# Optimization experiments

Hardware: AMD Instinct MI355X
Metric: run time of the kernel (lower is better)

## Reference

```python
import jax, jax.numpy as jnp
import numpy as np

DIM = 1024
HEADS = 16
HEAD_DIM = DIM // HEADS
MLP = 4 * DIM
EPS = 1e-5


def layer_norm(x, g, b):
    mu = jnp.mean(x, axis=-1, keepdims=True)
    var = jnp.var(x, axis=-1, keepdims=True)
    return (x - mu) * jax.lax.rsqrt(var + EPS) * g + b


def rope_cos_sin(n, d):
    inv_freq = 1.0 / (10000.0 ** (jnp.arange(0, d, 2, dtype=jnp.float32) / d))
    t = jnp.arange(n, dtype=jnp.float32)
    freqs = jnp.outer(t, inv_freq)          # [N, d/2]
    emb = jnp.concatenate([freqs, freqs], -1)  # [N, d]
    return jnp.cos(emb), jnp.sin(emb)


def rotate_half(x):
    x1, x2 = x[..., ::2], x[..., 1::2]
    return jnp.concatenate([-x2, x1], axis=-1)


def setup_inputs() -> dict:
    key = jax.random.key(0)
    ks = jax.random.split(key, 16)
    B, N = 2, 2048
    s = lambda fan_in: 1.0 / np.sqrt(fan_in)
    inp = {
        "x": jax.random.normal(ks[0], (B, N, DIM), jnp.float32),
        "t_emb": jax.random.normal(ks[1], (B, DIM), jnp.float32),
        "norm1_g": jnp.ones((DIM,), jnp.float32),
        "norm1_b": jnp.zeros((DIM,), jnp.float32),
        "Wq": jax.random.normal(ks[2], (DIM, DIM), jnp.float32) * s(DIM),
        "Wk": jax.random.normal(ks[3], (DIM, DIM), jnp.float32) * s(DIM),
        "Wv": jax.random.normal(ks[4], (DIM, DIM), jnp.float32) * s(DIM),
        "Wo": jax.random.normal(ks[5], (DIM, DIM), jnp.float32) * s(DIM),
        "norm2_g": jnp.ones((DIM,), jnp.float32),
        "norm2_b": jnp.zeros((DIM,), jnp.float32),
        "W1": jax.random.normal(ks[6], (DIM, MLP), jnp.float32) * s(DIM),
        "W2": jax.random.normal(ks[7], (MLP, DIM), jnp.float32) * s(MLP),
        "ada_W": jax.random.normal(ks[8], (DIM, 6 * DIM), jnp.float32) * s(DIM),
        "ada_b": jnp.zeros((6 * DIM,), jnp.float32),
    }
    return inp


def reference(x, t_emb, norm1_g, norm1_b, Wq, Wk, Wv, Wo,
              norm2_g, norm2_b, W1, W2, ada_W, ada_b):
    B, N, C = x.shape
    H, D = HEADS, HEAD_DIM
    scale = D ** -0.5

    mod = jax.nn.silu(t_emb) @ ada_W + ada_b          # [B, 6C]
    (shift_msa, scale_msa, gate_msa,
     shift_mlp, scale_mlp, gate_mlp) = jnp.split(mod, 6, axis=-1)

    xn = layer_norm(x, norm1_g, norm1_b) * (1 + scale_msa[:, None, :]) + shift_msa[:, None, :]

    q = (xn @ Wq).reshape(B, N, H, D).transpose(0, 2, 1, 3)  # [B,H,N,D]
    k = (xn @ Wk).reshape(B, N, H, D).transpose(0, 2, 1, 3)
    v = (xn @ Wv).reshape(B, N, H, D).transpose(0, 2, 1, 3)

    cos, sin = rope_cos_sin(N, D)                     # [N, D]
    q = q * cos + rotate_half(q) * sin
    k = k * cos + rotate_half(k) * sin

    attn = jnp.einsum('bhnd,bhmd->bhnm', q, k) * scale  # explicit O(N^2) scores
    attn = jax.nn.softmax(attn, axis=-1)
    out = jnp.einsum('bhnm,bhmd->bhnd', attn, v)

    out = out.transpose(0, 2, 1, 3).reshape(B, N, C) @ Wo
    x = x + gate_msa[:, None, :] * out

    xn = layer_norm(x, norm2_g, norm2_b) * (1 + scale_mlp[:, None, :]) + shift_mlp[:, None, :]
    mlp = jax.nn.gelu(xn @ W1, approximate=False) @ W2
    x = x + gate_mlp[:, None, :] * mlp
    return x
```

## Files before the change

### kernel.cpp

```cpp
#include <hip/hip_runtime.h>
#include <math.h>

#define BB    2
#define NN    2048
#define CDIM  1024
#define HEADS 16
#define HDIM  64
#define MLPD  4096
#define MODC  6144
#define EPSV  1e-5f
#define LOG2E 1.4426950408889634f
#define MSPLIT 16

typedef __attribute__((ext_vector_type(8))) short s8v;
typedef __attribute__((ext_vector_type(4))) float f4v;

__device__ inline unsigned short f2bf(float f) {
  union { float f; unsigned u; } v; v.f = f;
  unsigned r = v.u + 0x7FFFu + ((v.u >> 16) & 1u);
  return (unsigned short)(r >> 16);
}
__device__ inline float bf2f(unsigned short h) {
  union { unsigned u; float f; } v; v.u = ((unsigned)h) << 16;
  return v.f;
}

__global__ __launch_bounds__(256) void mod_part(
    const float* __restrict__ t_emb, const float* __restrict__ ada_W,
    float* __restrict__ part) {
  int j = blockIdx.x * 256 + threadIdx.x;
  int b = blockIdx.y, ks = blockIdx.z;
  __shared__ float st[64];
  if (threadIdx.x < 64) {
    float v = t_emb[b * CDIM + ks * 64 + threadIdx.x];
    st[threadIdx.x] = v / (1.0f + expf(-v));
  }
  __syncthreads();
  float acc = 0.f;
  const float* wp = ada_W + (size_t)(ks * 64) * MODC + j;
  #pragma unroll 8
  for (int i = 0; i < 64; ++i) acc += st[i] * wp[(size_t)i * MODC];
  part[((size_t)ks * BB + b) * MODC + j] = acc;
}

__global__ __launch_bounds__(256) void mod_reduce(
    const float* __restrict__ part, const float* __restrict__ ada_b,
    float* __restrict__ mod) {
  int idx = blockIdx.x * 256 + threadIdx.x;
  int b = idx / MODC, j = idx % MODC;
  float a = ada_b[j];
  #pragma unroll
  for (int s = 0; s < MSPLIT; ++s) a += part[((size_t)s * BB + b) * MODC + j];
  mod[(size_t)b * MODC + j] = a;
}

__device__ inline float wave_sum64(float v) {
  for (int o = 32; o > 0; o >>= 1) v += __shfl_down(v, o, 64);
  return v;
}

__global__ __launch_bounds__(256) void ln_mod_bf16(
    const float* __restrict__ x, const float* __restrict__ g,
    const float* __restrict__ bta, const float* __restrict__ mod,
    int shift_off, int scale_off, unsigned short* __restrict__ out) {
  int r = blockIdx.x;
  int b = r / NN;
  int t = threadIdx.x;
  const float* xr = x + (size_t)r * CDIM;
  float4 xv = ((const float4*)xr)[t];
  float s  = xv.x + xv.y + xv.z + xv.w;
  float s2 = xv.x*xv.x + xv.y*xv.y + xv.z*xv.z + xv.w*xv.w;
  __shared__ float ws1[4], ws2[4];
  float sw = wave_sum64(s), s2w = wave_sum64(s2);
  int lane = t & 63, wid = t >> 6;
  if (lane == 0) { ws1[wid] = sw; ws2[wid] = s2w; }
  __syncthreads();
  float mu  = (ws1[0] + ws1[1] + ws1[2] + ws1[3]) * (1.0f / CDIM);
  float var = (ws2[0] + ws2[1] + ws2[2] + ws2[3]) * (1.0f / CDIM) - mu * mu;
  float rstd = rsqrtf(var + EPSV);
  const float* mods = mod + (size_t)b * MODC;
  float4 gv = ((const float4*)g)[t];
  float4 bv = ((const float4*)bta)[t];
  float4 sc = ((const float4*)(mods + scale_off))[t];
  float4 sh = ((const float4*)(mods + shift_off))[t];
  ushort4 ov;
  ov.x = f2bf(((xv.x - mu) * rstd * gv.x + bv.x) * (1.0f + sc.x) + sh.x);
  ov.y = f2bf(((xv.y - mu) * rstd * gv.y + bv.y) * (1.0f + sc.y) + sh.y);
  ov.z = f2bf(((xv.z - mu) * rstd * gv.z + bv.z) * (1.0f + sc.z) + sh.z);
  ov.w = f2bf(((xv.w - mu) * rstd * gv.w + bv.w) * (1.0f + sc.w) + sh.w);
  ((ushort4*)(out + (size_t)r * CDIM))[t] = ov;
}

__global__ __launch_bounds__(256) void wcast_all(
    const float* __restrict__ Wq, const float* __restrict__ Wk,
    const float* __restrict__ Wv, const float* __restrict__ Wo,
    const float* __restrict__ W1, const float* __restrict__ W2,
    unsigned short* __restrict__ Wqkvt, unsigned short* __restrict__ Wot,
    unsigned short* __restrict__ W1t, unsigned short* __restrict__ W2t) {
  int bid = blockIdx.x;
  const float* W; unsigned short* Wt; int K, N, t;
  if (bid < 4096) {
    int m = bid >> 10;
    t = bid & 1023;
    K = CDIM; N = CDIM;
    W  = (m == 0) ? Wq : (m == 1) ? Wk : (m == 2) ? Wv : Wo;
    Wt = (m == 3) ? Wot : (Wqkvt + (size_t)m * CDIM * CDIM);
  } else if (bid < 8192) {
    t = bid - 4096; K = CDIM; N = MLPD; W = W1; Wt = W1t;
  } else {
    t = bid - 8192; K = MLPD; N = CDIM; W = W2; Wt = W2t;
  }
  int ntiles = N >> 5;
  int n0 = (t % ntiles) * 32, k0 = (t / ntiles) * 32;
  __shared__ float tile[32][33];
  int tx = threadIdx.x & 31, ty = threadIdx.x >> 5;
  #pragma unroll
  for (int p = 0; p < 4; ++p)
    tile[ty + p * 8][tx] = W[(size_t)(k0 + ty + p * 8) * N + n0 + tx];
  __syncthreads();
  #pragma unroll
  for (int p = 0; p < 4; ++p)
    Wt[(size_t)(n0 + ty + p * 8) * K + k0 + tx] = f2bf(tile[tx][ty + p * 8]);
}

__global__ __launch_bounds__(256) void mfma_gemm(
    const unsigned short* __restrict__ A,
    const unsigned short* __restrict__ Bt,
    int M, int N, int K,
    unsigned short* __restrict__ Ob, unsigned short* __restrict__ Ob2,
    unsigned short* __restrict__ Ob3, int mode) {
  __shared__ unsigned short As[128 * 32];
  __shared__ unsigned short Bs[128 * 32];
  int tid = threadIdx.x;
  int wave = tid >> 6, lane = tid & 63;
  int quad = lane >> 4, l15 = lane & 15;
  int m0 = blockIdx.y * 128, n0 = blockIdx.x * 128;
  int wm = (wave >> 1) * 64, wn = (wave & 1) * 64;

  f4v acc[4][4] = {};
  int srow = lane >> 2;
  int scol = (lane & 3) * 8;

  for (int k0 = 0; k0 < K; k0 += 32) {
    __syncthreads();
    #pragma unroll
    for (int s = 0; s < 2; ++s) {
      int inst = 2 * wave + s;
      const unsigned short* ga =
          A + (size_t)(m0 + inst * 16 + srow) * K + k0 + scol;
      __builtin_amdgcn_global_load_lds(
          (const __attribute__((address_space(1))) unsigned int*)(const void*)ga,
          (__attribute__((address_space(3))) unsigned int*)(void*)(As + inst * 512),
          16, 0, 0);
      const unsigned short* gb =
          Bt + (size_t)(n0 + inst * 16 + srow) * K + k0 + scol;
      __builtin_amdgcn_global_load_lds(
          (const __attribute__((address_space(1))) unsigned int*)(const void*)gb,
          (__attribute__((address_space(3))) unsigned int*)(void*)(Bs + inst * 512),
          16, 0, 0);
    }
    __syncthreads();

    s8v af[4], bf[4];
    #pragma unroll
    for (int i = 0; i < 4; ++i)
      af[i] = *(const s8v*)(As + ((wm + i * 16 + l15) * 32 + quad * 8));
    #pragma unroll
    for (int j = 0; j < 4; ++j)
      bf[j] = *(const s8v*)(Bs + ((wn + j * 16 + l15) * 32 + quad * 8));
    #pragma unroll
    for (int i = 0; i < 4; ++i)
      #pragma unroll
      for (int j = 0; j < 4; ++j)
        acc[i][j] = __builtin_amdgcn_mfma_f32_16x16x32_bf16(
            af[i], bf[j], acc[i][j], 0, 0, 0);
  }

  #pragma unroll
  for (int i = 0; i < 4; ++i) {
    int rbase = m0 + wm + i * 16 + quad * 4;
    #pragma unroll
    for (int j = 0; j < 4; ++j) {
      int c = n0 + wn + j * 16 + l15;
      #pragma unroll
      for (int rg = 0; rg < 4; ++rg) {
        int r = rbase + rg;
        float v = acc[i][j][rg];
        if (mode == 0) {
          unsigned short* dst = (c < 1024) ? Ob : ((c < 2048) ? Ob2 : Ob3);
          dst[(size_t)r * 1024 + (c & 1023)] = f2bf(v);
        } else {
          v = 0.5f * v * (1.0f + erff(v * 0.70710678118f));
          Ob[(size_t)r * N + c] = f2bf(v);
        }
      }
    }
  }
}

__global__ __launch_bounds__(1024) void mfma_gemm_res(
    const unsigned short* __restrict__ A,
    const unsigned short* __restrict__ Bt,
    int M, int N, int K,
    float* __restrict__ O0,
    const float* __restrict__ res, const float* __restrict__ mod,
    int gate_off) {
  __shared__ unsigned short SH[3 * 16384];
  int tid = threadIdx.x;
  int wave = tid >> 6, lane = tid & 63;
  int quad = lane >> 4, l15 = lane & 15;
  int m0 = blockIdx.y * 128, n0 = blockIdx.x * 128;
  int pos = wave & 7;
  int om = pos >> 1, on = pos & 1;
  int ks = wave >> 3;

  f4v acc[2][4] = {};

  int srow = lane >> 3;
  int ksrc = ((lane & 7) ^ (lane >> 3)) << 3;
  const int nt = K >> 6;

  #define STAGE_RES(T, BUF)                                                    \
    {                                                                          \
      int k0_ = (T) << 6;                                                      \
      unsigned short* dsta = SH + (BUF) * 16384 + wave * 512;                  \
      const unsigned short* ga =                                               \
          A + (size_t)(m0 + 8 * wave + srow) * K + k0_ + ksrc;                 \
      __builtin_amdgcn_global_load_lds(                                        \
          (const __attribute__((address_space(1))) unsigned int*)(const void*)ga, \
          (__attribute__((address_space(3))) unsigned int*)(void*)dsta,        \
          16, 0, 0);                                                           \
      const unsigned short* gb =                                               \
          Bt + (size_t)(n0 + 8 * wave + srow) * K + k0_ + ksrc;                \
      __builtin_amdgcn_global_load_lds(                                        \
          (const __attribute__((address_space(1))) unsigned int*)(const void*)gb, \
          (__attribute__((address_space(3))) unsigned int*)(void*)(dsta + 8192), \
          16, 0, 0);                                                           \
    }

  STAGE_RES(0, 0);
  STAGE_RES(1, 1);
  asm volatile("s_waitcnt vmcnt(2)" ::: "memory");
  __syncthreads();

  int kx = (ks * 32 + quad * 8) ^ ((l15 & 7) << 3);

  int rbuf = 0, sbuf = 2;
  for (int t = 0; t < nt; ++t) {
    if (t + 2 < nt) STAGE_RES(t + 2, sbuf);

    const unsigned short* base = SH + rbuf * 16384;
    s8v af[2], bf[4];
    #pragma unroll
    for (int i = 0; i < 2; ++i)
      af[i] = *(const s8v*)(base + (om * 32 + i * 16 + l15) * 64 + kx);
    #pragma unroll
    for (int j = 0; j < 4; ++j)
      bf[j] = *(const s8v*)(base + 8192 + (on * 64 + j * 16 + l15) * 64 + kx);
    #pragma unroll
    for (int i = 0; i < 2; ++i)
      #pragma unroll
      for (int j = 0; j < 4; ++j)
        acc[i][j] = __builtin_amdgcn_mfma_f32_16x16x32_bf16(
            af[i], bf[j], acc[i][j], 0, 0, 0);

    if (t + 2 < nt) {
      asm volatile("s_waitcnt vmcnt(2)" ::: "memory");
    } else if (t + 1 < nt) {
      asm volatile("s_waitcnt vmcnt(0)" ::: "memory");
    }
    __syncthreads();
    rbuf = (rbuf == 2) ? 0 : rbuf + 1;
    sbuf = (sbuf == 2) ? 0 : sbuf + 1;
  }
  #undef STAGE_RES

  float* red = (float*)SH;
  if (wave >= 8) {
    int rb = (wave - 8) * 2304 + lane * 36;
    #pragma unroll
    for (int i = 0; i < 2; ++i)
      #pragma unroll
      for (int j = 0; j < 4; ++j)
        *(f4v*)(red + rb + (i * 4 + j) * 4) = acc[i][j];
  }
  __syncthreads();
  if (wave < 8) {
    int rb = wave * 2304 + lane * 36;
    #pragma unroll
    for (int i = 0; i < 2; ++i)
      #pragma unroll
      for (int j = 0; j < 4; ++j)
        acc[i][j] += *(const f4v*)(red + rb + (i * 4 + j) * 4);
    #pragma unroll
    for (int i = 0; i < 2; ++i) {
      int rbase = m0 + om * 32 + i * 16 + quad * 4;
      #pragma unroll
      for (int j = 0; j < 4; ++j) {
        int c = n0 + on * 64 + j * 16 + l15;
        #pragma unroll
        for (int rg = 0; rg < 4; ++rg) {
          int r = rbase + rg;
          int bb2 = r >> 11;
          O0[(size_t)r * N + c] =
              res[(size_t)r * N + c] + mod[bb2 * MODC + gate_off + c] * acc[i][j][rg];
        }
      }
    }
  }
}

__global__ __launch_bounds__(256) void rope_qk(
    unsigned short* __restrict__ qb, const unsigned short* __restrict__ kb,
    unsigned short* __restrict__ kpack, float qscale) {
  int r = blockIdx.x;
  int b = r / NN, n = r % NN;
  int t = threadIdx.x;
  int isK = blockIdx.y;
  const unsigned short* src = isK ? kb : qb;
  float scale = isK ? 1.0f : qscale;
  __shared__ float row[CDIM];
  __shared__ float csv[32], snv[32];
  if (t < 32) {
    float invf = powf(10000.0f, -(float)t / 32.0f);
    float sn, cs;
    sincosf((float)n * invf, &sn, &cs);
    csv[t] = cs * scale; snv[t] = sn * scale;
  }
  const unsigned short* qr = src + (size_t)r * CDIM;
  ushort4 xv = ((const ushort4*)qr)[t];
  row[t * 4 + 0] = bf2f(xv.x);
  row[t * 4 + 1] = bf2f(xv.y);
  row[t * 4 + 2] = bf2f(xv.z);
  row[t * 4 + 3] = bf2f(xv.w);
  __syncthreads();
  unsigned short o[4];
  int c0 = t * 4;
  #pragma unroll
  for (int q4 = 0; q4 < 4; ++q4) {
    int c = c0 + q4;
    int h = c >> 6, d = c & 63;
    int i = d & 31;
    float rh = (d < 32) ? -row[h * 64 + 2 * d + 1] : row[h * 64 + 2 * (d - 32)];
    o[q4] = f2bf(row[c] * csv[i] + rh * snv[i]);
  }
  if (!isK) {
    ((ushort4*)(qb + (size_t)r * CDIM))[t] = make_ushort4(o[0], o[1], o[2], o[3]);
  } else {
    int h = c0 >> 6, d0 = c0 & 63;
    int half = d0 >> 5, quad = (d0 >> 3) & 3, j0 = d0 & 7;
    int bh = b * HEADS + h;
    int tt = n >> 6, kt = (n >> 4) & 3, l15 = n & 15;
    int lane = quad * 16 + l15;
    size_t off = ((((size_t)bh * 32 + tt) * 8 + kt * 2 + half) * 64 + lane) * 8 + j0;
    unsigned int lo = (unsigned)o[0] | ((unsigned)o[1] << 16);
    unsigned int hi = (unsigned)o[2] | ((unsigned)o[3] << 16);
    *(uint2*)(kpack + off) = make_uint2(lo, hi);
  }
}

__global__ __launch_bounds__(256) void vtrans_pack(
    const unsigned short* __restrict__ vrow, unsigned short* __restrict__ vpack) {
  int t = blockIdx.x;
  int bh = blockIdx.y;
  int b = bh >> 4, h = bh & 15;
  __shared__ unsigned short L[64 * 72];
  int tid = threadIdx.x;
  #pragma unroll
  for (int p = 0; p < 2; ++p) {
    int c = tid + p * 256;
    int key = c >> 3, dc = (c & 7) * 8;
    *(s8v*)(L + key * 72 + dc) =
        *(const s8v*)(vrow + (size_t)(b * NN + t * 64 + key) * CDIM + h * HDIM + dc);
  }
  __syncthreads();
  #pragma unroll
  for (int p = 0; p < 2; ++p) {
    int o = tid + p * 256;
    int f = o >> 6, lane = o & 63;
    int dt = f >> 1, half = f & 1, quad = lane >> 4, l15 = lane & 15;
    int d = dt * 16 + l15;
    unsigned short tmp[8];
    #pragma unroll
    for (int j = 0; j < 8; ++j) {
      int key = (j & 3) * 16 + half * 8 + quad * 2 + (j >> 2);
      tmp[j] = L[key * 72 + d];
    }
    *(s8v*)(vpack + ((((size_t)bh * 32 + t) * 8 + f) * 64 + lane) * 8) = *(s8v*)tmp;
  }
}

__global__ __launch_bounds__(256, 4) void fattn_pack(
    const unsigned short* __restrict__ qb,
    const unsigned short* __restrict__ kpack,
    const unsigned short* __restrict__ vpack,
    unsigned short* __restrict__ ob) {
  int bid = blockIdx.x;
  int qt = bid >> 5, bh = bid & 31;
  int b = bh >> 4, h = bh & 15;
  int tid = threadIdx.x;
  int wave = tid >> 6, lane = tid & 63;
  int quad = lane >> 4, l15 = lane & 15;

  __shared__ unsigned short Ps[4][16 * 72];

  int n0 = qt * 64;
  int qrow = n0 + wave * 16 + l15;
  s8v qf[2];
  {
    const unsigned short* qp = qb + (size_t)(b * NN + qrow) * CDIM + h * HDIM;
    qf[0] = *(const s8v*)(qp + quad * 8);
    qf[1] = *(const s8v*)(qp + 32 + quad * 8);
  }

  f4v acc[4] = {};
  float m_i[4], l_i[4];
  #pragma unroll
  for (int r = 0; r < 4; ++r) { m_i[r] = -1e30f; l_i[r] = 0.f; }

  const unsigned short* kbase = kpack + (size_t)bh * 32 * 4096 + lane * 8;
  const unsigned short* vbase = vpack + (size_t)bh * 32 * 4096 + lane * 8;
  unsigned short* Pw = Ps[wave];

  for (int t = 0; t < NN / 64; ++t) {
    const unsigned short* kt_ = kbase + (size_t)t * 4096;
    const unsigned short* vt_ = vbase + (size_t)t * 4096;
    s8v kf[8], vf[8];
    #pragma unroll
    for (int f = 0; f < 8; ++f) kf[f] = *(const s8v*)(kt_ + f * 512);
    #pragma unroll
    for (int f = 0; f < 8; ++f) vf[f] = *(const s8v*)(vt_ + f * 512);

    f4v s4[4] = {};
    #pragma unroll
    for (int kt = 0; kt < 4; ++kt) {
      s4[kt] = __builtin_amdgcn_mfma_f32_16x16x32_bf16(qf[0], kf[kt * 2], s4[kt], 0, 0, 0);
      s4[kt] = __builtin_amdgcn_mfma_f32_16x16x32_bf16(qf[1], kf[kt * 2 + 1], s4[kt], 0, 0, 0);
    }

    #pragma unroll
    for (int r = 0; r < 4; ++r) {
      float mv = fmaxf(fmaxf(s4[0][r], s4[1][r]), fmaxf(s4[2][r], s4[3][r]));
      #pragma unroll
      for (int msk = 1; msk < 16; msk <<= 1)
        mv = fmaxf(mv, __shfl_xor(mv, msk, 64));
      float mnew = fmaxf(m_i[r], mv);
      float alpha = __builtin_amdgcn_exp2f(m_i[r] - mnew);
      m_i[r] = mnew;
      float ls = 0.f;
      #pragma unroll
      for (int kt = 0; kt < 4; ++kt) {
        float p = __builtin_amdgcn_exp2f(s4[kt][r] - mnew);
        s4[kt][r] = p;
        ls += p;
      }
      l_i[r] = l_i[r] * alpha + ls;
      acc[0][r] *= alpha; acc[1][r] *= alpha;
      acc[2][r] *= alpha; acc[3][r] *= alpha;
    }

    #pragma unroll
    for (int r = 0; r < 4; ++r) {
      unsigned int lo = (__float_as_uint(s4[0][r]) >> 16) |
                        (__float_as_uint(s4[1][r]) & 0xffff0000u);
      unsigned int hi = (__float_as_uint(s4[2][r]) >> 16) |
                        (__float_as_uint(s4[3][r]) & 0xffff0000u);
      *(uint2*)(Pw + (quad * 4 + r) * 72 + l15 * 4) = make_uint2(lo, hi);
    }

    s8v pf0 = *(const s8v*)(Pw + l15 * 72 + quad * 8);
    s8v pf1 = *(const s8v*)(Pw + l15 * 72 + 32 + quad * 8);

    #pragma unroll
    for (int dt = 0; dt < 4; ++dt) {
      acc[dt] = __builtin_amdgcn_mfma_f32_16x16x32_bf16(pf0, vf[dt * 2], acc[dt], 0, 0, 0);
      acc[dt] = __builtin_amdgcn_mfma_f32_16x16x32_bf16(pf1, vf[dt * 2 + 1], acc[dt], 0, 0, 0);
    }
  }

  #pragma unroll
  for (int r = 0; r < 4; ++r) {
    float l = l_i[r];
    #pragma unroll
    for (int msk = 1; msk < 16; msk <<= 1)
      l += __shfl_xor(l, msk, 64);
    float inv = 1.0f / l;
    size_t row = (size_t)(b * NN + n0 + wave * 16 + quad * 4 + r);
    unsigned short* op = ob + row * CDIM + h * HDIM;
    #pragma unroll
    for (int dt = 0; dt < 4; ++dt)
      op[dt * 16 + l15] = f2bf(acc[dt][r] * inv);
  }
}

extern "C" void kernel_launch(void* const* d_in, const int* in_sizes, int n_in,
                              void* d_out, int out_size, void* d_ws, size_t ws_size,
                              hipStream_t stream) {
  const float* x    = (const float*)d_in[0];
  const float* temb = (const float*)d_in[1];
  const float* n1g  = (const float*)d_in[2];
  const float* n1b  = (const float*)d_in[3];
  const float* Wq   = (const float*)d_in[4];
  const float* Wk   = (const float*)d_in[5];
  const float* Wv   = (const float*)d_in[6];
  const float* Wo   = (const float*)d_in[7];
  const float* n2g  = (const float*)d_in[8];
  const float* n2b  = (const float*)d_in[9];
  const float* W1   = (const float*)d_in[10];
  const float* W2   = (const float*)d_in[11];
  const float* adaW = (const float*)d_in[12];
  const float* adab = (const float*)d_in[13];
  float* out = (float*)d_out;

  const size_t TOK = (size_t)BB * NN * CDIM;
  float* wsf = (float*)d_ws;
  float* mod     = wsf;
  float* modpart = wsf + 16384;
  unsigned short* tokb  = (unsigned short*)(wsf + 16384 + MSPLIT * BB * MODC);
  unsigned short* qb    = tokb + TOK;
  unsigned short* kb    = qb + TOK;
  unsigned short* kpack = kb + TOK;
  unsigned short* vpack = kpack + TOK;
  unsigned short* Wqkvt = vpack + TOK;
  unsigned short* Wot   = Wqkvt + 3 * CDIM * CDIM;
  unsigned short* W1t   = Wot + CDIM * CDIM;
  unsigned short* W2t   = W1t + CDIM * MLPD;
  unsigned short* h1b   = W2t + MLPD * CDIM;
  unsigned short* vrow  = h1b;
  float* x1 = (float*)qb;

  const int M = BB * NN;

  mod_part<<<dim3(MODC / 256, BB, MSPLIT), 256, 0, stream>>>(temb, adaW, modpart);
  mod_reduce<<<dim3(BB * MODC / 256), 256, 0, stream>>>(modpart, adab, mod);
  ln_mod_bf16<<<dim3(M), 256, 0, stream>>>(x, n1g, n1b, mod, 0, 1024, tokb);

  wcast_all<<<dim3(12288), 256, 0, stream>>>(
      Wq, Wk, Wv, Wo, W1, W2, Wqkvt, Wot, W1t, W2t);

  mfma_gemm<<<dim3(24, 32), 256, 0, stream>>>(
      tokb, Wqkvt, M, 3 * CDIM, CDIM, qb, kb, vrow, 0);

  rope_qk<<<dim3(M, 2), 256, 0, stream>>>(qb, kb, kpack, 0.125f * LOG2E);

  vtrans_pack<<<dim3(NN / 64, BB * HEADS), 256, 0, stream>>>(vrow, vpack);

  fattn_pack<<<dim3((NN / 64) * BB * HEADS), 256, 0, stream>>>(
      qb, kpack, vpack, tokb);

  mfma_gemm_res<<<dim3(CDIM / 128, M / 128), 1024, 0, stream>>>(
      tokb, Wot, M, CDIM, CDIM, x1, x, mod, 2048);

  ln_mod_bf16<<<dim3(M), 256, 0, stream>>>(x1, n2g, n2b, mod, 3072, 4096, tokb);

  mfma_gemm<<<dim3(MLPD / 128, M / 128), 256, 0, stream>>>(
      tokb, W1t, M, MLPD, CDIM, h1b, nullptr, nullptr, 1);

  mfma_gemm_res<<<dim3(CDIM / 128, M / 128), 1024, 0, stream>>>(
      h1b, W2t, M, CDIM, MLPD, out, x1, mod, 5120);
}
```

Before: 425.8 us.

## Split attention KV loop across two wave groups and merge partial softmax

Doubles the flash-attention block to 512 threads, with two groups of four waves each handling half of the key/value tiles for the same 64 query rows. Partial accumulators, running max and sum from the second group are written to shared memory and merged by the first group using rescaled online-softmax combination. This halves the serial KV loop per wave to expose more parallelism and latency hiding, at the cost of an extra shared-memory merge, two barriers, and higher register-pressure constraints from the launch bounds.

```diff
diff --git a/kernel.cpp b/kernel.cpp
--- a/kernel.cpp
+++ b/kernel.cpp
@@ -390,7 +390,7 @@
   }
 }
 
-__global__ __launch_bounds__(256, 4) void fattn_pack(
+__global__ __launch_bounds__(512, 8) void fattn_pack(
     const unsigned short* __restrict__ qb,
     const unsigned short* __restrict__ kpack,
     const unsigned short* __restrict__ vpack,
@@ -401,11 +401,14 @@
   int tid = threadIdx.x;
   int wave = tid >> 6, lane = tid & 63;
   int quad = lane >> 4, l15 = lane & 15;
-
-  __shared__ unsigned short Ps[4][16 * 72];
+  int qw = wave & 3;
+  int kvh = wave >> 2;
+
+  __shared__ float smem[6400];
+  unsigned short* Pw = (unsigned short*)smem + wave * (16 * 72);
 
   int n0 = qt * 64;
-  int qrow = n0 + wave * 16 + l15;
+  int qrow = n0 + qw * 16 + l15;
   s8v qf[2];
   {
     const unsigned short* qp = qb + (size_t)(b * NN + qrow) * CDIM + h * HDIM;
@@ -420,9 +423,9 @@
 
   const unsigned short* kbase = kpack + (size_t)bh * 32 * 4096 + lane * 8;
   const unsigned short* vbase = vpack + (size_t)bh * 32 * 4096 + lane * 8;
-  unsigned short* Pw = Ps[wave];
-
-  for (int t = 0; t < NN / 64; ++t) {
+
+  int t0 = kvh * 16;
+  for (int t = t0; t < t0 + 16; ++t) {
     const unsigned short* kt_ = kbase + (size_t)t * 4096;
     const unsigned short* vt_ = vbase + (size_t)t * 4096;
     s8v kf[8], vf[8];
@@ -478,18 +481,39 @@
     }
   }
 
-  #pragma unroll
-  for (int r = 0; r < 4; ++r) {
-    float l = l_i[r];
-    #pragma unroll
-    for (int msk = 1; msk < 16; msk <<= 1)
-      l += __shfl_xor(l, msk, 64);
-    float inv = 1.0f / l;
-    size_t row = (size_t)(b * NN + n0 + wave * 16 + quad * 4 + r);
-    unsigned short* op = ob + row * CDIM + h * HDIM;
+  __syncthreads();
+  if (kvh == 1) {
+    float* mb = smem + qw * (64 * 25) + lane * 25;
     #pragma unroll
     for (int dt = 0; dt < 4; ++dt)
-      op[dt * 16 + l15] = f2bf(acc[dt][r] * inv);
+      #pragma unroll
+      for (int r = 0; r < 4; ++r)
+        mb[dt * 4 + r] = acc[dt][r];
+    #pragma unroll
+    for (int r = 0; r < 4; ++r) { mb[16 + r] = m_i[r]; mb[20 + r] = l_i[r]; }
+  }
+  __syncthreads();
+  if (kvh == 0) {
+    const float* mb = smem + qw * (64 * 25) + lane * 25;
+    #pragma unroll
+    for (int r = 0; r < 4; ++r) {
+      float m2 = mb[16 + r], l2p = mb[20 + r];
+      float m = fmaxf(m_i[r], m2);
+      float a1 = __builtin_amdgcn_exp2f(m_i[r] - m);
+      float a2 = __builtin_amdgcn_exp2f(m2 - m);
+      float lp = l_i[r] * a1 + l2p * a2;
+      #pragma unroll
+      for (int msk = 1; msk < 16; msk <<= 1)
+        lp += __shfl_xor(lp, msk, 64);
+      float inv = 1.0f / lp;
+      size_t row = (size_t)(b * NN + n0 + qw * 16 + quad * 4 + r);
+      unsigned short* op = ob + row * CDIM + h * HDIM;
+      #pragma unroll
+      for (int dt = 0; dt < 4; ++dt) {
+        float v = (acc[dt][r] * a1 + mb[dt * 4 + r] * a2) * inv;
+        op[dt * 16 + l15] = f2bf(v);
+      }
+    }
   }
 }
 
@@ -545,7 +569,7 @@
 
   vtrans_pack<<<dim3(NN / 64, BB * HEADS), 256, 0, stream>>>(vrow, vpack);
 
-  fattn_pack<<<dim3((NN / 64) * BB * HEADS), 256, 0, stream>>>(
+  fattn_pack<<<dim3((NN / 64) * BB * HEADS), 512, 0, stream>>>(
       qb, kpack, vpack, tokb);
 
   mfma_gemm_res<<<dim3(CDIM / 128, M / 128), 1024, 0, stream>>>(
```

Result: slower. 470.4 us (+10.5%).

## Share K/V tiles across eight attention waves via double-buffered LDS async loads

Applied to the files above, without the earlier changes.

The flash-attention kernel now runs 512-thread blocks covering 128 query rows instead of 64. Each K/V tile is loaded once per block into LDS with global_load_lds, then read by all eight waves, instead of every wave fetching the full tile from global memory. The next tile is loaded into a second LDS buffer while the current one is being computed, with a wait and block barrier per iteration. This is meant to cut redundant global/L2 traffic and hide load latency. In exchange it adds about 51 KB of LDS per block and a barrier per tile, which may lower occupancy, and it halves the number of blocks.

```diff
diff --git a/kernel.cpp b/kernel.cpp
--- a/kernel.cpp
+++ b/kernel.cpp
@@ -390,7 +390,7 @@
   }
 }
 
-__global__ __launch_bounds__(256, 4) void fattn_pack(
+__global__ __launch_bounds__(512, 4) void fattn_pack(
     const unsigned short* __restrict__ qb,
     const unsigned short* __restrict__ kpack,
     const unsigned short* __restrict__ vpack,
@@ -402,9 +402,10 @@
   int wave = tid >> 6, lane = tid & 63;
   int quad = lane >> 4, l15 = lane & 15;
 
-  __shared__ unsigned short Ps[4][16 * 72];
-
-  int n0 = qt * 64;
+  __shared__ unsigned short smem[16384 + 8 * 1152];
+  unsigned short* Pw = smem + 16384 + wave * 1152;
+
+  int n0 = qt * 128;
   int qrow = n0 + wave * 16 + l15;
   s8v qf[2];
   {
@@ -418,18 +419,36 @@
   #pragma unroll
   for (int r = 0; r < 4; ++r) { m_i[r] = -1e30f; l_i[r] = 0.f; }
 
-  const unsigned short* kbase = kpack + (size_t)bh * 32 * 4096 + lane * 8;
-  const unsigned short* vbase = vpack + (size_t)bh * 32 * 4096 + lane * 8;
-  unsigned short* Pw = Ps[wave];
-
+  const unsigned short* ksrc = kpack + (size_t)bh * 131072 + wave * 512 + lane * 8;
+  const unsigned short* vsrc = vpack + (size_t)bh * 131072 + wave * 512 + lane * 8;
+
+  #define STAGE_ATT(T, BUF)                                                    \
+    {                                                                          \
+      __builtin_amdgcn_global_load_lds(                                        \
+          (const __attribute__((address_space(1))) unsigned int*)(const void*)(ksrc + (size_t)(T) * 4096), \
+          (__attribute__((address_space(3))) unsigned int*)(void*)(smem + (BUF) * 8192 + wave * 512), \
+          16, 0, 0);                                                           \
+      __builtin_amdgcn_global_load_lds(                                        \
+          (const __attribute__((address_space(1))) unsigned int*)(const void*)(vsrc + (size_t)(T) * 4096), \
+          (__attribute__((address_space(3))) unsigned int*)(void*)(smem + (BUF) * 8192 + 4096 + wave * 512), \
+          16, 0, 0);                                                           \
+    }
+
+  STAGE_ATT(0, 0);
+  asm volatile("s_waitcnt vmcnt(0)" ::: "memory");
+  __syncthreads();
+
+  int buf = 0;
   for (int t = 0; t < NN / 64; ++t) {
-    const unsigned short* kt_ = kbase + (size_t)t * 4096;
-    const unsigned short* vt_ = vbase + (size_t)t * 4096;
+    if (t + 1 < NN / 64) STAGE_ATT(t + 1, buf ^ 1);
+
+    const unsigned short* kb_ = smem + buf * 8192 + lane * 8;
+    const unsigned short* vb_ = kb_ + 4096;
     s8v kf[8], vf[8];
     #pragma unroll
-    for (int f = 0; f < 8; ++f) kf[f] = *(const s8v*)(kt_ + f * 512);
-    #pragma unroll
-    for (int f = 0; f < 8; ++f) vf[f] = *(const s8v*)(vt_ + f * 512);
+    for (int f = 0; f < 8; ++f) kf[f] = *(const s8v*)(kb_ + f * 512);
+    #pragma unroll
+    for (int f = 0; f < 8; ++f) vf[f] = *(const s8v*)(vb_ + f * 512);
 
     f4v s4[4] = {};
     #pragma unroll
@@ -476,7 +495,14 @@
       acc[dt] = __builtin_amdgcn_mfma_f32_16x16x32_bf16(pf0, vf[dt * 2], acc[dt], 0, 0, 0);
       acc[dt] = __builtin_amdgcn_mfma_f32_16x16x32_bf16(pf1, vf[dt * 2 + 1], acc[dt], 0, 0, 0);
     }
-  }
+
+    if (t + 1 < NN / 64) {
+      asm volatile("s_waitcnt vmcnt(0)" ::: "memory");
+      __syncthreads();
+      buf ^= 1;
+    }
+  }
+  #undef STAGE_ATT
 
   #pragma unroll
   for (int r = 0; r < 4; ++r) {
@@ -545,7 +571,7 @@
 
   vtrans_pack<<<dim3(NN / 64, BB * HEADS), 256, 0, stream>>>(vrow, vpack);
 
-  fattn_pack<<<dim3((NN / 64) * BB * HEADS), 256, 0, stream>>>(
+  fattn_pack<<<dim3((NN / 128) * BB * HEADS), 512, 0, stream>>>(
       qb, kpack, vpack, tokb);
 
   mfma_gemm_res<<<dim3(CDIM / 128, M / 128), 1024, 0, stream>>>(
```

New measurement: 427.6 us. About the same (+0.4%).
